# Performance work log

Hardware: AMD Instinct MI355X
Metric: run time of the kernel (lower is better)

The kernel has to match this reference:

```python
import jax, jax.numpy as jnp
import numpy as np

B, V, E, D_IN, D_OUT = 8, 10000, 160000, 128, 128
BN_EPS = 1e-5


def setup_inputs() -> dict:
    key = jax.random.key(0)
    ks = jax.random.split(key, 8)
    X = jax.random.normal(ks[0], (B, V, D_IN), dtype=jnp.float32)
    edge_attr = jax.random.normal(ks[1], (B, E), dtype=jnp.float32)
    W_node = jax.random.normal(ks[2], (D_OUT, D_IN), dtype=jnp.float32) * (1.0 / np.sqrt(D_IN))
    W_edge = jax.random.normal(ks[3], (D_OUT, 1), dtype=jnp.float32)
    W_self = jax.random.normal(ks[4], (D_OUT, D_IN), dtype=jnp.float32) * (1.0 / np.sqrt(D_IN))
    b_self = jax.random.normal(ks[5], (D_OUT,), dtype=jnp.float32) * 0.01
    gamma = jnp.ones((D_OUT,), dtype=jnp.float32)
    beta = jnp.zeros((D_OUT,), dtype=jnp.float32)
    edge_index = jax.random.randint(ks[6], (E, 2), 0, V, dtype=jnp.int32)
    return {"X": X, "edge_attr": edge_attr, "W_node": W_node, "W_edge": W_edge,
            "W_self": W_self, "b_self": b_self, "gamma": gamma, "beta": beta,
            "edge_index": edge_index}


def reference(X, edge_attr, W_node, W_edge, W_self, b_self, gamma, beta, edge_index):
    src = edge_index[:, 0]  # [E]
    dst = edge_index[:, 1]  # [E]
    # self-loop linear
    H = jnp.einsum('bvf,of->bvo', X, W_self) + b_self  # [B,V,D_OUT]
    # fused gather -> per-edge message -> scatter-add
    msg = jnp.einsum('bef,of->beo', X[:, src, :], W_node)  # [B,E,D_OUT]
    msg = msg + edge_attr[:, :, None] * W_edge[:, 0][None, None, :]
    aggregated = jnp.zeros_like(H).at[:, dst, :].add(msg)
    H = H + aggregated
    # BatchNorm1d over channel dim (training mode, biased variance over B*V)
    mean = jnp.mean(H, axis=(0, 1))
    var = jnp.var(H, axis=(0, 1))
    Hn = (H - mean) * jax.lax.rsqrt(var + BN_EPS) * gamma + beta
    return jax.nn.relu(Hn)
```

## Files before the change

kernel.cpp:

```cpp
#include <hip/hip_runtime.h>

#define B_ 8
#define V_ 10000
#define E_ 160000
#define DIN 128
#define DOUT 128
#define M_ (B_*V_)
#define NINV (1.0f/80000.0f)
#define BN_EPS 1e-5f

#define GEMM_BLOCKS 2500
#define CAP 64

#define WS_CNT     0
#define WS_SUM     10000
#define WS_SUMSQ   10128
#define WS_ZERO_UNITS 10256
#define WS_S       10256
#define WS_SSRC    90256
#define WS_EAS     730256
#define WS_HH      730256
#define WS_WPK     5850256
#define WS_XH      5866640
#define WS_AH      10986640

typedef __attribute__((ext_vector_type(2))) _Float16 half2_t;
typedef __attribute__((ext_vector_type(4))) _Float16 half4_t;
typedef __attribute__((ext_vector_type(8))) _Float16 half8_t;
typedef __attribute__((ext_vector_type(4))) float f32x4;

__device__ inline half2_t i2h(unsigned i) {
    half2_t h; __builtin_memcpy(&h, &i, 4); return h;
}
__device__ inline unsigned h2i(half2_t h) {
    unsigned i; __builtin_memcpy(&i, &h, 4); return i;
}

__global__ __launch_bounds__(256) void prep_kernel(
    const float* __restrict__ X, _Float16* __restrict__ Xh,
    const float* __restrict__ Wself, const float* __restrict__ Wnode,
    _Float16* __restrict__ Wpk,
    const int* __restrict__ EI, const float* __restrict__ EA,
    int* __restrict__ cnt, int* __restrict__ ssrc, float* __restrict__ EAs)
{
    const int blk = blockIdx.x;
    const int t = threadIdx.x;
    if (blk < 10000) {
        int idx = blk * 256 + t;
        float4 v = ((const float4*)X)[idx];
        half4_t o = { (_Float16)v.x, (_Float16)v.y, (_Float16)v.z, (_Float16)v.w };
        ((half4_t*)Xh)[idx] = o;
    } else if (blk < 10016) {
        int g = (blk - 10000) * 256 + t;
        int pair = g >> 6;
        int lane = g & 63;
        int ks = pair >> 3;
        int nt = pair & 7;
        int o = nt * 16 + (lane & 15);
        int k = ks * 32 + (lane >> 4) * 8;
        const float* wsrc = (k < 128) ? (Wself + o * 128 + k)
                                      : (Wnode + o * 128 + (k - 128));
        _Float16* dst = Wpk + ((size_t)pair * 64 + lane) * 8;
#pragma unroll
        for (int j = 0; j < 8; ++j) dst[j] = (_Float16)wsrc[j];
    } else {
        int e = (blk - 10016) * 256 + t;
        int src = EI[2 * e];
        int dst = EI[2 * e + 1];
        int slot = atomicAdd(&cnt[dst], 1);
        if (slot < CAP) {
            int p = dst * CAP + slot;
            ssrc[p] = src;
            float4 v0, v1;
            v0.x = EA[0 * E_ + e]; v0.y = EA[1 * E_ + e];
            v0.z = EA[2 * E_ + e]; v0.w = EA[3 * E_ + e];
            v1.x = EA[4 * E_ + e]; v1.y = EA[5 * E_ + e];
            v1.z = EA[6 * E_ + e]; v1.w = EA[7 * E_ + e];
            *(float4*)(EAs + (size_t)p * 8) = v0;
            *(float4*)(EAs + (size_t)p * 8 + 4) = v1;
        }
    }
}

__global__ __launch_bounds__(256) void gather_kernel(
    const _Float16* __restrict__ Xh, const float* __restrict__ EAs,
    const int* __restrict__ cnt, const int* __restrict__ ssrc,
    _Float16* __restrict__ Ah, float* __restrict__ S)
{
    const int b = blockIdx.x & 7;
    const int dblk = blockIdx.x >> 3;
    const int w = threadIdx.x >> 6;
    const int lane = threadIdx.x & 63;
    const int q = lane >> 4;
    const int sl = lane & 15;
    const int d = dblk * 4 + w;
    const int wid = b * V_ + d;
    const int deg = min(cnt[d], CAP);
    const int k0 = d * CAP;
    const _Float16* Xb = Xh + (size_t)b * V_ * DIN + sl * 8;
    half2_t a0 = (half2_t)0, a1 = (half2_t)0, a2 = (half2_t)0, a3 = (half2_t)0;
    float ea = 0.0f;
    {
        int msrc = 0;
        if (lane < deg) {
            msrc = ssrc[k0 + lane];
            ea = EAs[(size_t)(k0 + lane) * 8 + b];
        }
        int j = 0;
        for (; j + 16 <= deg; j += 16) {
#pragma unroll
            for (int u = 0; u < 4; ++u) {
                int s = __shfl(msrc, j + u * 4 + q);
                uint4 v = *(const uint4*)(Xb + (size_t)s * DIN);
                a0 += i2h(v.x); a1 += i2h(v.y); a2 += i2h(v.z); a3 += i2h(v.w);
            }
        }
        for (; j + 4 <= deg; j += 4) {
            int s = __shfl(msrc, j + q);
            uint4 v = *(const uint4*)(Xb + (size_t)s * DIN);
            a0 += i2h(v.x); a1 += i2h(v.y); a2 += i2h(v.z); a3 += i2h(v.w);
        }
        if (j < deg) {
            int s = __shfl(msrc, j + q);
            if (j + q < deg) {
                uint4 v = *(const uint4*)(Xb + (size_t)s * DIN);
                a0 += i2h(v.x); a1 += i2h(v.y); a2 += i2h(v.z); a3 += i2h(v.w);
            }
        }
    }
#pragma unroll
    for (int off = 32; off >= 16; off >>= 1) {
        a0 += i2h(__shfl_down(h2i(a0), off));
        a1 += i2h(__shfl_down(h2i(a1), off));
        a2 += i2h(__shfl_down(h2i(a2), off));
        a3 += i2h(__shfl_down(h2i(a3), off));
    }
    for (int off = 32; off; off >>= 1) ea += __shfl_down(ea, off);
    if (lane == 0) S[wid] = ea;
    if (lane < 16) {
        uint4 o;
        o.x = h2i(a0); o.y = h2i(a1); o.z = h2i(a2); o.w = h2i(a3);
        *(uint4*)(Ah + (size_t)wid * DIN + sl * 8) = o;
    }
}

__global__ __launch_bounds__(256, 4) void gemm_stats_kernel(
    const _Float16* __restrict__ Xh, const _Float16* __restrict__ Ah,
    const _Float16* __restrict__ Wpk, const float* __restrict__ S,
    const float* __restrict__ bself, const float* __restrict__ wedge,
    _Float16* __restrict__ Hh, float* __restrict__ gsum,
    float* __restrict__ gsumsq)
{
    __shared__ _Float16 aLds[8192];
    const int t = threadIdx.x;
    const int wave = t >> 6;
    const int lane = t & 63;
    const int quad = lane >> 4;
    const int ln = lane & 15;
    const int rowbase = blockIdx.x * 32;

#pragma unroll
    for (int i = 0; i < 4; ++i) {
        int c = wave * 4 + i;
        int row = 2 * c + (lane >> 5);
        int col16 = lane & 31;
        int scol = col16 ^ (row & 7);
        int m = rowbase + row;
        const _Float16* src = (scol < 16)
            ? Xh + (size_t)m * DIN + scol * 8
            : Ah + (size_t)m * DIN + (scol - 16) * 8;
        __builtin_amdgcn_global_load_lds(
            (const __attribute__((address_space(1))) void*)src,
            (__attribute__((address_space(3))) void*)
                ((char*)aLds + (size_t)c * 1024),
            16, 0, 0);
    }

    f32x4 acc[2][2];
#pragma unroll
    for (int mt = 0; mt < 2; ++mt)
#pragma unroll
        for (int ntl = 0; ntl < 2; ++ntl) acc[mt][ntl] = (f32x4){0.f,0.f,0.f,0.f};

    __syncthreads();

#pragma unroll
    for (int ks = 0; ks < 8; ++ks) {
        half8_t b0 = *(const half8_t*)(
            Wpk + ((size_t)(ks * 8 + wave * 2 + 0) * 64 + lane) * 8);
        half8_t b1 = *(const half8_t*)(
            Wpk + ((size_t)(ks * 8 + wave * 2 + 1) * 64 + lane) * 8);
#pragma unroll
        for (int mt = 0; mt < 2; ++mt) {
            int row = mt * 16 + ln;
            int u = (ks * 4 + quad) ^ (row & 7);
            half8_t af = *(const half8_t*)(
                (const char*)aLds + (size_t)row * 512 + (size_t)u * 16);
            acc[mt][0] = __builtin_amdgcn_mfma_f32_16x16x32_f16(af, b0, acc[mt][0], 0, 0, 0);
            acc[mt][1] = __builtin_amdgcn_mfma_f32_16x16x32_f16(af, b1, acc[mt][1], 0, 0, 0);
        }
    }

    float bs[2], we[2];
#pragma unroll
    for (int ntl = 0; ntl < 2; ++ntl) {
        int c = wave * 32 + ntl * 16 + ln;
        bs[ntl] = bself[c];
        we[ntl] = wedge[c];
    }
    float psum[2] = {0.f, 0.f}, psq[2] = {0.f, 0.f};

#pragma unroll
    for (int mt = 0; mt < 2; ++mt) {
        const int rb = rowbase + mt * 16 + quad * 4;
        float sv[4];
#pragma unroll
        for (int r = 0; r < 4; ++r) sv[r] = S[rb + r];
#pragma unroll
        for (int r = 0; r < 4; ++r) {
            _Float16* Hr = Hh + (size_t)(rb + r) * DOUT + wave * 32 + ln;
#pragma unroll
            for (int ntl = 0; ntl < 2; ++ntl) {
                float h = acc[mt][ntl][r] + bs[ntl] + sv[r] * we[ntl];
                Hr[ntl * 16] = (_Float16)h;
                psum[ntl] += h;
                psq[ntl] += h * h;
            }
        }
    }
#pragma unroll
    for (int ntl = 0; ntl < 2; ++ntl) {
        psum[ntl] += __shfl_down(psum[ntl], 32);
        psum[ntl] += __shfl_down(psum[ntl], 16);
        psq[ntl]  += __shfl_down(psq[ntl], 32);
        psq[ntl]  += __shfl_down(psq[ntl], 16);
    }
    if (lane < 16) {
#pragma unroll
        for (int ntl = 0; ntl < 2; ++ntl) {
            int c = wave * 32 + ntl * 16 + lane;
            atomicAdd(&gsum[c], psum[ntl]);
            atomicAdd(&gsumsq[c], psq[ntl]);
        }
    }
}

__global__ __launch_bounds__(256) void norm_relu_kernel(
    const _Float16* __restrict__ Hh, float* __restrict__ H,
    const float* __restrict__ gsum, const float* __restrict__ gsumsq,
    const float* __restrict__ gamma, const float* __restrict__ beta)
{
    const int total = M_ * DOUT / 8;
    for (int idx = blockIdx.x * 256 + threadIdx.x; idx < total;
         idx += gridDim.x * 256) {
        int o8 = (idx & 15) * 8;
        float4 s0 = *(const float4*)(gsum + o8);
        float4 s1 = *(const float4*)(gsum + o8 + 4);
        float4 q0 = *(const float4*)(gsumsq + o8);
        float4 q1 = *(const float4*)(gsumsq + o8 + 4);
        float4 g0 = *(const float4*)(gamma + o8);
        float4 g1 = *(const float4*)(gamma + o8 + 4);
        float4 b0 = *(const float4*)(beta + o8);
        float4 b1 = *(const float4*)(beta + o8 + 4);
        float sc[8], sh[8];
        float svv[8] = {s0.x, s0.y, s0.z, s0.w, s1.x, s1.y, s1.z, s1.w};
        float qv[8] = {q0.x, q0.y, q0.z, q0.w, q1.x, q1.y, q1.z, q1.w};
        float gv[8] = {g0.x, g0.y, g0.z, g0.w, g1.x, g1.y, g1.z, g1.w};
        float bv[8] = {b0.x, b0.y, b0.z, b0.w, b1.x, b1.y, b1.z, b1.w};
#pragma unroll
        for (int j = 0; j < 8; ++j) {
            float mean = svv[j] * NINV;
            float rstd = rsqrtf(qv[j] * NINV - mean * mean + BN_EPS);
            sc[j] = gv[j] * rstd;
            sh[j] = bv[j] - mean * sc[j];
        }
        half8_t hv = ((const half8_t*)Hh)[idx];
        float4 o0, o1;
        o0.x = fmaxf((float)hv[0] * sc[0] + sh[0], 0.0f);
        o0.y = fmaxf((float)hv[1] * sc[1] + sh[1], 0.0f);
        o0.z = fmaxf((float)hv[2] * sc[2] + sh[2], 0.0f);
        o0.w = fmaxf((float)hv[3] * sc[3] + sh[3], 0.0f);
        o1.x = fmaxf((float)hv[4] * sc[4] + sh[4], 0.0f);
        o1.y = fmaxf((float)hv[5] * sc[5] + sh[5], 0.0f);
        o1.z = fmaxf((float)hv[6] * sc[6] + sh[6], 0.0f);
        o1.w = fmaxf((float)hv[7] * sc[7] + sh[7], 0.0f);
        ((float4*)H)[idx * 2]     = o0;
        ((float4*)H)[idx * 2 + 1] = o1;
    }
}

extern "C" void kernel_launch(void* const* d_in, const int* in_sizes, int n_in,
                              void* d_out, int out_size, void* d_ws, size_t ws_size,
                              hipStream_t stream)
{
    const float* X      = (const float*)d_in[0];
    const float* EA     = (const float*)d_in[1];
    const float* Wnode  = (const float*)d_in[2];
    const float* Wedge  = (const float*)d_in[3];
    const float* Wself  = (const float*)d_in[4];
    const float* bself  = (const float*)d_in[5];
    const float* gamma  = (const float*)d_in[6];
    const float* beta   = (const float*)d_in[7];
    const int*   EI     = (const int*)d_in[8];

    int*   wsI    = (int*)d_ws;
    float* wsF    = (float*)d_ws;
    int*   cnt    = wsI + WS_CNT;
    float* gsum   = wsF + WS_SUM;
    float* gsumsq = wsF + WS_SUMSQ;
    float* S      = wsF + WS_S;
    int*   ssrc   = wsI + WS_SSRC;
    float* EAs    = wsF + WS_EAS;
    _Float16* Hh  = (_Float16*)(wsI + WS_HH);
    _Float16* Wpk = (_Float16*)(wsI + WS_WPK);
    _Float16* Xh  = (_Float16*)(wsI + WS_XH);
    _Float16* Ah  = (_Float16*)(wsI + WS_AH);
    float* H      = (float*)d_out;

    hipMemsetAsync(d_ws, 0, (size_t)WS_ZERO_UNITS * 4, stream);

    prep_kernel<<<10641, 256, 0, stream>>>(X, Xh, Wself, Wnode, Wpk, EI, EA,
                                           cnt, ssrc, EAs);

    gather_kernel<<<M_ / 4, 256, 0, stream>>>(Xh, EAs, cnt, ssrc, Ah, S);

    gemm_stats_kernel<<<GEMM_BLOCKS, 256, 0, stream>>>(Xh, Ah, Wpk, S, bself,
                                                       Wedge, Hh, gsum, gsumsq);

    norm_relu_kernel<<<2048, 256, 0, stream>>>(Hh, H, gsum, gsumsq, gamma, beta);
}
```

Baseline: 233.9 us.

## Retile GEMM into 64-row, 64-column halves with weights staged in LDS

Each GEMM block now covers 64 rows and one 64-column half of the output (two blocks per row tile) instead of 32 rows by all 128 columns. The packed weight slice is copied into LDS asynchronously alongside the A tile, so B fragments come from LDS rather than global memory. Each wave now does 4 M-tiles by 1 N-tile. The trade-off is that the A tile (X and aggregated rows) is loaded twice, once per column half. LDS use rises to 64 KB and the occupancy hint drops to 2 blocks per CU.

```diff
diff --git a/kernel.cpp b/kernel.cpp
--- a/kernel.cpp
+++ b/kernel.cpp
@@ -144,24 +144,38 @@
     }
 }
 
-__global__ __launch_bounds__(256, 4) void gemm_stats_kernel(
+__global__ __launch_bounds__(256, 2) void gemm_stats_kernel(
     const _Float16* __restrict__ Xh, const _Float16* __restrict__ Ah,
     const _Float16* __restrict__ Wpk, const float* __restrict__ S,
     const float* __restrict__ bself, const float* __restrict__ wedge,
     _Float16* __restrict__ Hh, float* __restrict__ gsum,
     float* __restrict__ gsumsq)
 {
-    __shared__ _Float16 aLds[8192];
+    __shared__ _Float16 wlds[16384];
+    __shared__ _Float16 aLds[16384];
     const int t = threadIdx.x;
     const int wave = t >> 6;
     const int lane = t & 63;
     const int quad = lane >> 4;
     const int ln = lane & 15;
-    const int rowbase = blockIdx.x * 32;
-
-#pragma unroll
-    for (int i = 0; i < 4; ++i) {
-        int c = wave * 4 + i;
+    const int rblk = blockIdx.x >> 1;
+    const int nb   = blockIdx.x & 1;
+    const int rowbase = rblk * 64;
+
+#pragma unroll
+    for (int i = 0; i < 8; ++i) {
+        int c = i * 4 + wave;
+        int gp = i * 8 + nb * 4 + wave;
+        __builtin_amdgcn_global_load_lds(
+            (const __attribute__((address_space(1))) void*)
+                ((const char*)Wpk + (size_t)gp * 1024 + lane * 16),
+            (__attribute__((address_space(3))) void*)
+                ((char*)wlds + (size_t)c * 1024),
+            16, 0, 0);
+    }
+#pragma unroll
+    for (int i = 0; i < 8; ++i) {
+        int c = wave * 8 + i;
         int row = 2 * c + (lane >> 5);
         int col16 = lane & 31;
         int scol = col16 ^ (row & 7);
@@ -176,72 +190,51 @@
             16, 0, 0);
     }
 
-    f32x4 acc[2][2];
-#pragma unroll
-    for (int mt = 0; mt < 2; ++mt)
-#pragma unroll
-        for (int ntl = 0; ntl < 2; ++ntl) acc[mt][ntl] = (f32x4){0.f,0.f,0.f,0.f};
+    f32x4 acc[4];
+#pragma unroll
+    for (int mt = 0; mt < 4; ++mt) acc[mt] = (f32x4){0.f, 0.f, 0.f, 0.f};
 
     __syncthreads();
 
 #pragma unroll
     for (int ks = 0; ks < 8; ++ks) {
-        half8_t b0 = *(const half8_t*)(
-            Wpk + ((size_t)(ks * 8 + wave * 2 + 0) * 64 + lane) * 8);
-        half8_t b1 = *(const half8_t*)(
-            Wpk + ((size_t)(ks * 8 + wave * 2 + 1) * 64 + lane) * 8);
-#pragma unroll
-        for (int mt = 0; mt < 2; ++mt) {
+        half8_t bfr = *(const half8_t*)(wlds + (size_t)(ks * 4 + wave) * 512 + lane * 8);
+#pragma unroll
+        for (int mt = 0; mt < 4; ++mt) {
             int row = mt * 16 + ln;
             int u = (ks * 4 + quad) ^ (row & 7);
             half8_t af = *(const half8_t*)(
                 (const char*)aLds + (size_t)row * 512 + (size_t)u * 16);
-            acc[mt][0] = __builtin_amdgcn_mfma_f32_16x16x32_f16(af, b0, acc[mt][0], 0, 0, 0);
-            acc[mt][1] = __builtin_amdgcn_mfma_f32_16x16x32_f16(af, b1, acc[mt][1], 0, 0, 0);
-        }
-    }
-
-    float bs[2], we[2];
-#pragma unroll
-    for (int ntl = 0; ntl < 2; ++ntl) {
-        int c = wave * 32 + ntl * 16 + ln;
-        bs[ntl] = bself[c];
-        we[ntl] = wedge[c];
-    }
-    float psum[2] = {0.f, 0.f}, psq[2] = {0.f, 0.f};
-
-#pragma unroll
-    for (int mt = 0; mt < 2; ++mt) {
+            acc[mt] = __builtin_amdgcn_mfma_f32_16x16x32_f16(af, bfr, acc[mt], 0, 0, 0);
+        }
+    }
+
+    const int c = nb * 64 + wave * 16 + ln;
+    const float bs = bself[c];
+    const float we = wedge[c];
+    float psum = 0.0f, psq = 0.0f;
+
+#pragma unroll
+    for (int mt = 0; mt < 4; ++mt) {
         const int rb = rowbase + mt * 16 + quad * 4;
         float sv[4];
 #pragma unroll
         for (int r = 0; r < 4; ++r) sv[r] = S[rb + r];
 #pragma unroll
         for (int r = 0; r < 4; ++r) {
-            _Float16* Hr = Hh + (size_t)(rb + r) * DOUT + wave * 32 + ln;
-#pragma unroll
-            for (int ntl = 0; ntl < 2; ++ntl) {
-                float h = acc[mt][ntl][r] + bs[ntl] + sv[r] * we[ntl];
-                Hr[ntl * 16] = (_Float16)h;
-                psum[ntl] += h;
-                psq[ntl] += h * h;
-            }
-        }
-    }
-#pragma unroll
-    for (int ntl = 0; ntl < 2; ++ntl) {
-        psum[ntl] += __shfl_down(psum[ntl], 32);
-        psum[ntl] += __shfl_down(psum[ntl], 16);
-        psq[ntl]  += __shfl_down(psq[ntl], 32);
-        psq[ntl]  += __shfl_down(psq[ntl], 16);
-    }
+            float h = acc[mt][r] + bs + sv[r] * we;
+            Hh[(size_t)(rb + r) * DOUT + c] = (_Float16)h;
+            psum += h;
+            psq += h * h;
+        }
+    }
+    psum += __shfl_down(psum, 32);
+    psum += __shfl_down(psum, 16);
+    psq  += __shfl_down(psq, 32);
+    psq  += __shfl_down(psq, 16);
     if (lane < 16) {
-#pragma unroll
-        for (int ntl = 0; ntl < 2; ++ntl) {
-            int c = wave * 32 + ntl * 16 + lane;
-            atomicAdd(&gsum[c], psum[ntl]);
-            atomicAdd(&gsumsq[c], psq[ntl]);
-        }
+        atomicAdd(&gsum[c], psum);
+        atomicAdd(&gsumsq[c], psq);
     }
 }
 
```

After: 201.7 us. 1.16x faster.
